# Performance work log

Measured on AMD Instinct MI355X. Metric: run time of the kernel, lower is better.

## Reference

```python
import jax, jax.numpy as jnp
import numpy as np

D_MODEL = 1024
NHEAD = 16
D_K = D_MODEL // NHEAD
CHUNK = 256


def setup_inputs() -> dict:
    key = jax.random.key(0)
    ks = jax.random.split(key, 11)
    S, B = 4096, 4
    inp = {
        "query": jax.random.normal(ks[0], (S, B, D_MODEL), dtype=jnp.float32),
        "key": jax.random.normal(ks[1], (S, B, D_MODEL), dtype=jnp.float32),
        "value": jax.random.normal(ks[2], (S, B, D_MODEL), dtype=jnp.float32),
        # nn.Linear params: y = x @ W.T + b
        "Wq": jax.random.normal(ks[3], (D_MODEL, D_MODEL), dtype=jnp.float32) * 0.02,
        "bq": jnp.zeros((D_MODEL,), dtype=jnp.float32),
        "Wk": jax.random.normal(ks[4], (D_MODEL, D_MODEL), dtype=jnp.float32) * 0.02,
        "bk": jnp.zeros((D_MODEL,), dtype=jnp.float32),
        "Wv": jax.random.normal(ks[5], (D_MODEL, D_MODEL), dtype=jnp.float32) * 0.02,
        "bv": jnp.zeros((D_MODEL,), dtype=jnp.float32),
        "Wo": jax.random.normal(ks[6], (D_MODEL, D_MODEL), dtype=jnp.float32) * 0.02,
        "bo": jnp.zeros((D_MODEL,), dtype=jnp.float32),
    }
    return inp


def _split_heads(x, B):
    # (S, B, D) -> (B, H, S, d_k)
    S = x.shape[0]
    return x.reshape(S, B, NHEAD, D_K).transpose(1, 2, 0, 3)


def reference(query, key, value, Wq, bq, Wk, bk, Wv, bv, Wo, bo):
    S, B, _ = query.shape
    n_chunks = S // CHUNK  # S assumed divisible by CHUNK

    q = _split_heads(query @ Wq.T + bq, B)  # (B,H,S,dk)
    k = _split_heads(key @ Wk.T + bk, B)
    v = _split_heads(value @ Wv.T + bv, B)

    # Block-diagonal attention: softmax is strictly within each chunk.
    qc = q.reshape(B, NHEAD, n_chunks, CHUNK, D_K)
    kc = k.reshape(B, NHEAD, n_chunks, CHUNK, D_K)
    vc = v.reshape(B, NHEAD, n_chunks, CHUNK, D_K)

    scale = 1.0 / np.sqrt(D_K).astype(np.float32)
    scores = jnp.einsum("bhncd,bhnkd->bhnck", qc, kc) * scale  # (B,H,n,C,C)
    probs = jax.nn.softmax(scores, axis=-1)
    out = jnp.einsum("bhnck,bhnkd->bhncd", probs, vc)  # (B,H,n,C,dk)

    # (B,H,S,dk) -> (S,B,H*dk)
    out = out.reshape(B, NHEAD, S, D_K).transpose(2, 0, 1, 3).reshape(S, B, D_MODEL)
    return out @ Wo.T + bo
```

## Files before the change

### kernel.cpp

```cpp
#include <hip/hip_runtime.h>
#include <hip/hip_bf16.h>


namespace {

constexpr int kSeq = 4096, kB = 4, kDm = 1024, kNh = 16, kDk = 64, kChk = 256;
constexpr int kMr = kSeq * kB;
constexpr float kLog2e = 1.44269504088896340736f;

typedef __attribute__((ext_vector_type(8))) short bf16x8;
typedef __attribute__((ext_vector_type(4))) short bf16x4;
typedef __attribute__((ext_vector_type(4))) float f32x4;
typedef __attribute__((ext_vector_type(8))) unsigned short u16x8;
typedef __attribute__((ext_vector_type(4))) unsigned short u16x4;
typedef __attribute__((ext_vector_type(4))) unsigned u32x4;

#define AS1 __attribute__((address_space(1)))
#define AS3 __attribute__((address_space(3)))

__device__ __forceinline__ unsigned short f2bf(float x) {
  union { float f; unsigned u; } v; v.f = x;
  unsigned r = v.u + 0x7fffu + ((v.u >> 16) & 1u);
  return (unsigned short)(r >> 16);
}
__device__ __forceinline__ unsigned cvtpk(float lo, float hi) {
  unsigned r;
  asm("v_cvt_pk_bf16_f32 %0, %1, %2" : "=v"(r) : "v"(lo), "v"(hi));
  return r;
}
__device__ __forceinline__ int swz(int bo) { return bo ^ ((bo >> 3) & 0x70); }

__device__ __forceinline__ f32x4 mfma16x16(bf16x4 a, bf16x4 b, f32x4 c) {
#if __has_builtin(__builtin_amdgcn_mfma_f32_16x16x16bf16_1k)
  return __builtin_amdgcn_mfma_f32_16x16x16bf16_1k(a, b, c, 0, 0, 0);
#else
  asm volatile("v_mfma_f32_16x16x16_bf16 %0, %1, %2, %0\n\ts_nop 4"
               : "+v"(c) : "v"(a), "v"(b));
  return c;
#endif
}

__global__ __launch_bounds__(256) void cvt4(const float* __restrict__ s0,
                                            const float* __restrict__ s1,
                                            const float* __restrict__ s2,
                                            const float* __restrict__ s3,
                                            unsigned short* __restrict__ dst) {
  int i = blockIdx.x * 256 + threadIdx.x;
  int t = i >> 18;
  int j = i & 0x3ffff;
  const float* s = (t == 0) ? s0 : (t == 1) ? s1 : (t == 2) ? s2 : s3;
  f32x4 v = *(const f32x4*)(s + (size_t)j * 4);
  u16x4 o;
  o[0] = f2bf(v[0]); o[1] = f2bf(v[1]); o[2] = f2bf(v[2]); o[3] = f2bf(v[3]);
  *(u16x4*)(dst + (size_t)i * 4) = o;
}

__global__ __launch_bounds__(1024, 4) void gemm_qkv8(
    const float* __restrict__ qf, const float* __restrict__ kf,
    const float* __restrict__ vf, const unsigned short* __restrict__ Wcat,
    const float* __restrict__ bq, const float* __restrict__ bk,
    const float* __restrict__ bv, unsigned short* __restrict__ dst, float sQ) {
  constexpr int K = kDm, nkt = K / 64;
  __shared__ unsigned short sh[65536];
  const int tid = (int)threadIdx.x;
  const int l = tid & 63;
  const int l15 = l & 15, l4 = l >> 4, l7 = l15 & 7;
  const int wid = tid >> 6;
  const int wm = wid >> 2, wn = wid & 3;
  const int bid = (int)blockIdx.x;
  const int xcd = bid & 7, idx = bid >> 3;
  const int rbi = xcd * 8 + (idx & 7);
  const int cbi = idx >> 3;
  const int mat = cbi >> 2, ccol = (cbi & 3) * 256;
  const float* bp = (mat == 0) ? bq : (mat == 1) ? bk : bv;
  const float scale = (mat == 0) ? sQ : 1.0f;
  const float* Ain = (mat == 0) ? qf : (mat == 1) ? kf : vf;
  unsigned short* out = dst + (size_t)mat * kMr * kDm;

  const int ar = tid >> 3, ac = tid & 7;
  const float* gA = Ain + (size_t)(rbi * 256 + ar) * K + ac * 8;
  const int awp = (ac ^ (ar & 7)) * 8;
  const int srow = tid >> 3;
  const int g16 = (tid & 7) ^ (srow & 7);
  const unsigned short* gB = Wcat + (size_t)(cbi * 256 + srow) * K + g16 * 8;
  const int ldsbase = (tid & ~63) * 8;

  auto stageB = [&](int T, int h) {
    const unsigned short* s = gB + (size_t)h * (128 * K) + T * 64;
    unsigned short* d = sh + 32768 + ((T & 1) * 2 + h) * 8192 + ldsbase;
    __builtin_amdgcn_global_load_lds((const AS1 unsigned int*)s, (AS3 unsigned int*)d, 16, 0, 0);
  };
  auto loadA = [&](f32x4* r, int T, int h) {
    const float* s = gA + (size_t)h * (128 * K) + T * 64;
    r[0] = *(const f32x4*)s;
    r[1] = *(const f32x4*)(s + 4);
  };
  auto writeA = [&](const f32x4* r, int T, int h) {
    unsigned short* d = sh + ((T & 1) * 2 + h) * 8192 + ar * 64;
    u32x4 w = {cvtpk(r[0][0], r[0][1]), cvtpk(r[0][2], r[0][3]),
               cvtpk(r[1][0], r[1][1]), cvtpk(r[1][2], r[1][3])};
    *(u32x4*)(d + awp) = w;
  };

  f32x4 acc[4][4] = {};
  f32x4 a0[2], a1[2];
  bf16x8 bfr[4];

  loadA(a0, 0, 0); loadA(a1, 0, 1);
  stageB(0, 0); stageB(0, 1);
  stageB(1, 0); stageB(1, 1);
  writeA(a0, 0, 0); writeA(a1, 0, 1);
  asm volatile("s_waitcnt lgkmcnt(0)" ::: "memory");
  asm volatile("s_waitcnt vmcnt(2)" ::: "memory");
  __builtin_amdgcn_s_barrier();

  for (int it = 0; it < nkt / 2; ++it) {
#pragma unroll
    for (int tt = 0; tt < 2; ++tt) {
      const int T = 2 * it + tt;
      const unsigned short* Asl = sh + (tt * 2 + (wm >> 1)) * 8192;
      const unsigned short* Bsl = sh + 32768 + (tt * 2 + (wn >> 1)) * 8192;
      const int arow0 = (wm & 1) * 64;
      const int brow0 = (wn & 1) * 64;
#pragma unroll
      for (int p = 0; p < 4; ++p) {
        const int kk = p >> 1, mfh = p & 1;
        bf16x8 af[2];
        const int sc = ((kk * 4 + l4) ^ l7) * 8;
        if (mfh == 0) {
#pragma unroll
          for (int nf = 0; nf < 4; ++nf)
            bfr[nf] = *(const bf16x8*)&Bsl[(brow0 + nf * 16 + l15) * 64 + sc];
        }
#pragma unroll
        for (int i = 0; i < 2; ++i)
          af[i] = *(const bf16x8*)&Asl[(arow0 + mfh * 32 + i * 16 + l15) * 64 + sc];
        if (p == 0 && T + 1 < nkt) loadA(a0, T + 1, 0);
        if (p == 1 && T + 1 < nkt) loadA(a1, T + 1, 1);
        if (p == 3) {
          if (T + 2 < nkt) { stageB(T + 2, 0); stageB(T + 2, 1); }
          if (T + 1 < nkt) {
            writeA(a0, T + 1, 0);
            writeA(a1, T + 1, 1);
          }
        }
        __builtin_amdgcn_s_barrier();
        __builtin_amdgcn_s_setprio(1);
#pragma unroll
        for (int i = 0; i < 2; ++i)
#pragma unroll
          for (int nf = 0; nf < 4; ++nf)
            acc[mfh * 2 + i][nf] =
                __builtin_amdgcn_mfma_f32_16x16x32_bf16(af[i], bfr[nf], acc[mfh * 2 + i][nf], 0, 0, 0);
        __builtin_amdgcn_s_setprio(0);
        if (p == 3) {
          asm volatile("s_waitcnt lgkmcnt(0)" ::: "memory");
          if (T + 1 == nkt - 1)
            asm volatile("s_waitcnt vmcnt(0)" ::: "memory");
        }
        __builtin_amdgcn_s_barrier();
      }
    }
  }

#pragma unroll
  for (int mf = 0; mf < 4; ++mf)
#pragma unroll
    for (int nf = 0; nf < 4; ++nf) {
      int col = wn * 64 + nf * 16 + l15;
      float bvv = bp[ccol + col];
      int grpc = col >> 6;
      int c16 = (col & 63) >> 3, pos = col & 7;
      unsigned p01 = cvtpk((acc[mf][nf][0] + bvv) * scale, (acc[mf][nf][1] + bvv) * scale);
      unsigned p23 = cvtpk((acc[mf][nf][2] + bvv) * scale, (acc[mf][nf][3] + bvv) * scale);
      unsigned short ev[4] = {(unsigned short)p01, (unsigned short)(p01 >> 16),
                              (unsigned short)p23, (unsigned short)(p23 >> 16)};
#pragma unroll
      for (int j = 0; j < 4; ++j) {
        int tl = wm * 64 + mf * 16 + l4 * 4 + j;
        int grp = (tl & 3) * 4 + grpc;
        int u = (tl >> 2) * 8 + c16;
        int byte = (grp * 8192 + u * 16 + pos * 2) ^ (((u >> 3) & 7) << 4);
        *(unsigned short*)((char*)sh + byte) = ev[j];
      }
    }
  __syncthreads();
  {
    int inner = tid & 63, grp = tid >> 6;
    int b2 = grp >> 2, hl = grp & 3;
    int h = (cbi & 3) * 4 + hl;
    unsigned short* po = out + ((size_t)(b2 * kNh + h) * kSeq + rbi * 64) * kDk;
#pragma unroll
    for (int i = 0; i < 8; ++i) {
      int u = i * 64 + inner;
      int byte = (grp * 8192 + u * 16) ^ (((u >> 3) & 7) << 4);
      u16x8 v = *(const u16x8*)((const char*)sh + byte);
      *(u16x8*)(po + u * 8) = v;
    }
  }
}

__global__ __launch_bounds__(512, 2) void gemm_o8(const unsigned short* __restrict__ Aw,
                                                  const unsigned short* __restrict__ Bw,
                                                  const float* __restrict__ bias,
                                                  float* __restrict__ Cp) {
  constexpr int K = kDm, nkt = K / 64;
  __shared__ unsigned short sh[65536];
  const int tid = (int)threadIdx.x;
  const int l = tid & 63;
  const int l15 = l & 15, l4 = l >> 4, l7 = l15 & 7;
  const int wid = tid >> 6, wm = wid >> 2, wn = wid & 3, wn1 = wn & 1;
  const int bid = (int)blockIdx.x;
  const int xcd = bid & 7, idx = bid >> 3;
  const int rbi = xcd * 8 + (idx & 7);
  const int cbi = idx >> 3;
  const int rb = rbi * 256, cb = cbi * 256;

  const int srow = tid >> 3;
  const int g16 = (tid & 7) ^ (srow & 7);
  size_t abase[2][2];
#pragma unroll
  for (int h = 0; h < 2; ++h)
#pragma unroll
    for (int i = 0; i < 2; ++i) {
      int t = rb + h * 128 + srow + 64 * i;
      abase[h][i] = ((size_t)((t & 3) * kNh) * kSeq + (t >> 2)) * kDk + g16 * 8;
    }
  const unsigned short* gB = Bw + (size_t)(cb + srow) * K + g16 * 8;
  const int ldsbase = (tid & ~63) * 8;

  auto stageA = [&](int T, int h) {
    unsigned short* d = sh + ((T & 1) * 2 + h) * 8192 + ldsbase;
    size_t ko = (size_t)T * ((size_t)kSeq * kDk);
    __builtin_amdgcn_global_load_lds((const AS1 unsigned int*)(Aw + abase[h][0] + ko),
                                     (AS3 unsigned int*)d, 16, 0, 0);
    __builtin_amdgcn_global_load_lds((const AS1 unsigned int*)(Aw + abase[h][1] + ko),
                                     (AS3 unsigned int*)(d + 4096), 16, 0, 0);
  };
  auto stageB = [&](int T, int h) {
    const unsigned short* s = gB + (size_t)h * (128 * K) + T * 64;
    unsigned short* d = sh + 32768 + ((T & 1) * 2 + h) * 8192 + ldsbase;
    __builtin_amdgcn_global_load_lds((const AS1 unsigned int*)s, (AS3 unsigned int*)d, 16, 0, 0);
    __builtin_amdgcn_global_load_lds((const AS1 unsigned int*)(s + 64 * K),
                                     (AS3 unsigned int*)(d + 4096), 16, 0, 0);
  };

  f32x4 acc[8][4] = {};
  bf16x8 bfr[4];

  stageB(0, 0); stageB(0, 1);
  stageA(0, 0); stageA(0, 1);
  stageB(1, 0); stageB(1, 1);
  asm volatile("s_waitcnt vmcnt(4)" ::: "memory");
  __builtin_amdgcn_s_barrier();

  for (int it = 0; it < nkt / 2; ++it) {
#pragma unroll
    for (int tt = 0; tt < 2; ++tt) {
      const int T = 2 * it + tt;
      const unsigned short* Asl = sh + (tt * 2 + wm) * 8192;
      const unsigned short* Bsl = sh + 32768 + (tt * 2 + (wn >> 1)) * 8192;
#pragma unroll
      for (int p = 0; p < 4; ++p) {
        const int kk = p >> 1, mfh = p & 1;
        bf16x8 af[4];
        const int sc = ((kk * 4 + l4) ^ l7) * 8;
        if (mfh == 0) {
#pragma unroll
          for (int nf = 0; nf < 4; ++nf)
            bfr[nf] = *(const bf16x8*)&Bsl[(wn1 * 64 + nf * 16 + l15) * 64 + sc];
        }
#pragma unroll
        for (int i = 0; i < 4; ++i)
          af[i] = *(const bf16x8*)&Asl[(mfh * 64 + i * 16 + l15) * 64 + sc];
        if (p == 0 && T + 1 < nkt) stageA(T + 1, 0);
        if (p == 1 && T + 1 < nkt) stageA(T + 1, 1);
        if (p == 3 && T + 2 < nkt) { stageB(T + 2, 0); stageB(T + 2, 1); }
        __builtin_amdgcn_s_barrier();
        __builtin_amdgcn_s_setprio(1);
#pragma unroll
        for (int i = 0; i < 4; ++i)
#pragma unroll
          for (int nf = 0; nf < 4; ++nf)
            acc[mfh * 4 + i][nf] =
                __builtin_amdgcn_mfma_f32_16x16x32_bf16(af[i], bfr[nf], acc[mfh * 4 + i][nf], 0, 0, 0);
        __builtin_amdgcn_s_setprio(0);
        if (p == 3 && T + 1 < nkt) {
          if (T + 2 < nkt) asm volatile("s_waitcnt vmcnt(4)" ::: "memory");
          else             asm volatile("s_waitcnt vmcnt(0)" ::: "memory");
        }
        __builtin_amdgcn_s_barrier();
      }
    }
  }

#pragma unroll
  for (int nf = 0; nf < 4; ++nf) {
    int col = cb + wn * 64 + nf * 16 + l15;
    float bvv = bias[col];
#pragma unroll
    for (int mf = 0; mf < 8; ++mf) {
      int row0 = rb + wm * 128 + mf * 16 + l4 * 4;
#pragma unroll
      for (int j = 0; j < 4; ++j)
        Cp[(size_t)(row0 + j) * kDm + col] = acc[mf][nf][j] + bvv;
    }
  }
}

__global__ __launch_bounds__(256) void attn_blkdiag(const unsigned short* __restrict__ qw,
                                                    const unsigned short* __restrict__ kw,
                                                    const unsigned short* __restrict__ vw,
                                                    unsigned short* __restrict__ ow) {
  __shared__ unsigned short Kl[64 * 64];
  __shared__ unsigned short Vt[64 * 64];
  const int tid = (int)threadIdx.x;
  const int w = tid >> 6, l = tid & 63;
  const int l15 = l & 15, l4 = l >> 4;
  const int bid0 = (int)blockIdx.x;
  const int bid = (bid0 & 7) * 256 + (bid0 >> 3);
  const int hf = bid & 1, c = (bid >> 1) & 15, bh = bid >> 5;
  const size_t base = ((size_t)bh * kSeq + c * kChk) * kDk;
  const unsigned short* qp = qw + base + (size_t)hf * 128 * kDk;
  const unsigned short* kp = kw + base;
  const unsigned short* vp = vw + base;

  bf16x8 q[2][2];
#pragma unroll
  for (int m = 0; m < 2; ++m)
#pragma unroll
    for (int kk = 0; kk < 2; ++kk)
      q[m][kk] = *(const bf16x8*)(qp + (w * 32 + m * 16 + l15) * 64 + kk * 32 + l4 * 8);

  float mst[2] = {-1e30f, -1e30f}, lst[2] = {0.f, 0.f};
  f32x4 oacc[2][4] = {};

  const int r = tid >> 2, c0 = (tid & 3) * 16;
  u16x8 kr0, kr1, vr0, vr1;
  {
    const unsigned short* kt = kp + tid * 16;
    kr0 = *(const u16x8*)kt; kr1 = *(const u16x8*)(kt + 8);
    const unsigned short* vt = vp + tid * 16;
    vr0 = *(const u16x8*)vt; vr1 = *(const u16x8*)(vt + 8);
  }

  for (int kb = 0; kb < 4; ++kb) {
    __syncthreads();
    {
      int bo = r * 128 + c0 * 2;
      *(u16x8*)((char*)Kl + swz(bo)) = kr0;
      *(u16x8*)((char*)Kl + swz(bo + 16)) = kr1;
#pragma unroll
      for (int j = 0; j < 8; ++j) {
        *(unsigned short*)((char*)Vt + swz((c0 + j) * 128 + r * 2)) = vr0[j];
        *(unsigned short*)((char*)Vt + swz((c0 + 8 + j) * 128 + r * 2)) = vr1[j];
      }
    }
    __syncthreads();
    if (kb < 3) {
      const unsigned short* kt = kp + (kb + 1) * (64 * kDk) + tid * 16;
      kr0 = *(const u16x8*)kt; kr1 = *(const u16x8*)(kt + 8);
      const unsigned short* vt = vp + (kb + 1) * (64 * kDk) + tid * 16;
      vr0 = *(const u16x8*)vt; vr1 = *(const u16x8*)(vt + 8);
    }

    f32x4 sacc[4][2] = {};
    __builtin_amdgcn_s_setprio(1);
#pragma unroll
    for (int kk = 0; kk < 2; ++kk) {
      bf16x8 kf[4];
#pragma unroll
      for (int kn = 0; kn < 4; ++kn) {
        int bo = (kn * 16 + l15) * 128 + (kk * 32 + l4 * 8) * 2;
        kf[kn] = *(const bf16x8*)((const char*)Kl + swz(bo));
      }
#pragma unroll
      for (int kn = 0; kn < 4; ++kn)
#pragma unroll
        for (int m = 0; m < 2; ++m)
          sacc[kn][m] = __builtin_amdgcn_mfma_f32_16x16x32_bf16(kf[kn], q[m][kk], sacc[kn][m], 0, 0, 0);
    }
    __builtin_amdgcn_s_setprio(0);

    unsigned pw[2][4][2];
    float cbq[2][4];
#pragma unroll
    for (int m = 0; m < 2; ++m) {
      float rm = -1e30f;
#pragma unroll
      for (int kn = 0; kn < 4; ++kn)
#pragma unroll
        for (int j = 0; j < 4; ++j) rm = fmaxf(rm, sacc[kn][m][j]);
      rm = fmaxf(rm, __shfl_xor(rm, 16, 64));
      rm = fmaxf(rm, __shfl_xor(rm, 32, 64));
      float mn = fmaxf(mst[m], rm);
      float corr = exp2f(mst[m] - mn);
      mst[m] = mn;
      float rs = 0.f;
#pragma unroll
      for (int kn = 0; kn < 4; ++kn) {
#pragma unroll
        for (int j = 0; j < 4; ++j) {
          float p = exp2f(sacc[kn][m][j] - mn);
          sacc[kn][m][j] = p;
          rs += p;
        }
        pw[m][kn][0] = cvtpk(sacc[kn][m][0], sacc[kn][m][1]);
        pw[m][kn][1] = cvtpk(sacc[kn][m][2], sacc[kn][m][3]);
      }
      rs += __shfl_xor(rs, 16, 64);
      rs += __shfl_xor(rs, 32, 64);
      lst[m] = lst[m] * corr + rs;
#pragma unroll
      for (int j = 0; j < 4; ++j) cbq[m][j] = __shfl(corr, l4 * 4 + j, 64);
#pragma unroll
      for (int n = 0; n < 4; ++n)
#pragma unroll
        for (int j = 0; j < 4; ++j) oacc[m][n][j] *= cbq[m][j];
    }

    __builtin_amdgcn_s_setprio(1);
#pragma unroll
    for (int kn = 0; kn < 4; ++kn) {
      bf16x4 vf[4];
#pragma unroll
      for (int n = 0; n < 4; ++n) {
        int bo = (n * 16 + l15) * 128 + (kn * 16 + l4 * 4) * 2;
        vf[n] = *(const bf16x4*)((const char*)Vt + swz(bo));
      }
#pragma unroll
      for (int m = 0; m < 2; ++m) {
        union { unsigned u[2]; bf16x4 h; } pk;
        pk.u[0] = pw[m][kn][0]; pk.u[1] = pw[m][kn][1];
#pragma unroll
        for (int n = 0; n < 4; ++n)
          oacc[m][n] = mfma16x16(pk.h, vf[n], oacc[m][n]);
      }
    }
    __builtin_amdgcn_s_setprio(0);
  }

  unsigned short* op = ow + base + (size_t)hf * 128 * kDk;
#pragma unroll
  for (int m = 0; m < 2; ++m) {
    float inv = 1.f / lst[m];
#pragma unroll
    for (int j = 0; j < 4; ++j) {
      float ib = __shfl(inv, l4 * 4 + j, 64);
      int srow = w * 32 + m * 16 + l4 * 4 + j;
#pragma unroll
      for (int n = 0; n < 4; ++n)
        op[(size_t)srow * 64 + n * 16 + l15] = f2bf(oacc[m][n][j] * ib);
    }
  }
}

}

extern "C" void kernel_launch(void* const* d_in, const int* in_sizes, int n_in,
                              void* d_out, int out_size, void* d_ws, size_t ws_size,
                              hipStream_t stream) {
  const float* query = (const float*)d_in[0];
  const float* key   = (const float*)d_in[1];
  const float* value = (const float*)d_in[2];
  const float* Wq = (const float*)d_in[3];
  const float* bq = (const float*)d_in[4];
  const float* Wk = (const float*)d_in[5];
  const float* bk = (const float*)d_in[6];
  const float* Wv = (const float*)d_in[7];
  const float* bv = (const float*)d_in[8];
  const float* Wo = (const float*)d_in[9];
  const float* bo = (const float*)d_in[10];

  const float sQ = 0.125f * kLog2e;

  const size_t wsz = (size_t)kDm * kDm;
  const size_t tsz = (size_t)kMr * kDm;
  unsigned short* wsp = (unsigned short*)d_ws;
  unsigned short* wqb = wsp;
  unsigned short* wob = wqb + 3 * wsz;
  unsigned short* qws = wqb + 4 * wsz;
  unsigned short* kws = qws + tsz;
  unsigned short* vws = kws + tsz;
  unsigned short* aws = vws + tsz;

  const size_t need = (4 * wsz + 4 * tsz) * 2;
  if (ws_size < need) return;

  cvt4<<<dim3(4096), dim3(256), 0, stream>>>(Wq, Wk, Wv, Wo, wqb);
  gemm_qkv8<<<dim3(768), dim3(1024), 0, stream>>>(query, key, value, wqb,
                                                  bq, bk, bv, qws, sQ);
  attn_blkdiag<<<dim3(2048), 256, 0, stream>>>(qws, kws, vws, aws);
  gemm_o8<<<dim3(256), dim3(512), 0, stream>>>(aws, wob, bo, (float*)d_out);
}
```

Before: 242.1 us.

## Prefetch QKV A-tiles two steps ahead; run output GEMM with 16 waves

In the QKV GEMM, fp32 A-tile register loads now go two k-steps ahead using two alternating register sets, with vmcnt waits adjusted to match, so global load latency gets more time to hide. The output GEMM moves from 512 to 1024 threads per block, and each wave now owns a 64x64 sub-tile instead of 128x64. That cuts per-thread accumulators and loads per stage to raise wave-level parallelism. The costs are more registers held in the QKV kernel, and tighter register limits plus more barrier participants in the output GEMM.

```diff
diff --git a/kernel.cpp b/kernel.cpp
--- a/kernel.cpp
+++ b/kernel.cpp
@@ -103,13 +103,14 @@
   };
 
   f32x4 acc[4][4] = {};
-  f32x4 a0[2], a1[2];
+  f32x4 s0h0[2], s0h1[2], s1h0[2], s1h1[2];
   bf16x8 bfr[4];
 
-  loadA(a0, 0, 0); loadA(a1, 0, 1);
+  loadA(s0h0, 0, 0); loadA(s0h1, 0, 1);
+  loadA(s1h0, 1, 0); loadA(s1h1, 1, 1);
   stageB(0, 0); stageB(0, 1);
   stageB(1, 0); stageB(1, 1);
-  writeA(a0, 0, 0); writeA(a1, 0, 1);
+  writeA(s0h0, 0, 0); writeA(s0h1, 0, 1);
   asm volatile("s_waitcnt lgkmcnt(0)" ::: "memory");
   asm volatile("s_waitcnt vmcnt(2)" ::: "memory");
   __builtin_amdgcn_s_barrier();
@@ -135,13 +136,13 @@
 #pragma unroll
         for (int i = 0; i < 2; ++i)
           af[i] = *(const bf16x8*)&Asl[(arow0 + mfh * 32 + i * 16 + l15) * 64 + sc];
-        if (p == 0 && T + 1 < nkt) loadA(a0, T + 1, 0);
-        if (p == 1 && T + 1 < nkt) loadA(a1, T + 1, 1);
+        if (p == 0 && T + 2 < nkt) loadA(tt == 0 ? s0h0 : s1h0, T + 2, 0);
+        if (p == 1 && T + 2 < nkt) loadA(tt == 0 ? s0h1 : s1h1, T + 2, 1);
         if (p == 3) {
           if (T + 2 < nkt) { stageB(T + 2, 0); stageB(T + 2, 1); }
           if (T + 1 < nkt) {
-            writeA(a0, T + 1, 0);
-            writeA(a1, T + 1, 1);
+            writeA(tt == 0 ? s1h0 : s0h0, T + 1, 0);
+            writeA(tt == 0 ? s1h1 : s0h1, T + 1, 1);
           }
         }
         __builtin_amdgcn_s_barrier();
@@ -155,8 +156,10 @@
         __builtin_amdgcn_s_setprio(0);
         if (p == 3) {
           asm volatile("s_waitcnt lgkmcnt(0)" ::: "memory");
-          if (T + 1 == nkt - 1)
-            asm volatile("s_waitcnt vmcnt(0)" ::: "memory");
+          if (T + 1 < nkt) {
+            if (T + 2 < nkt) asm volatile("s_waitcnt vmcnt(6)" ::: "memory");
+            else             asm volatile("s_waitcnt vmcnt(0)" ::: "memory");
+          }
         }
         __builtin_amdgcn_s_barrier();
       }
@@ -200,16 +203,17 @@
   }
 }
 
-__global__ __launch_bounds__(512, 2) void gemm_o8(const unsigned short* __restrict__ Aw,
-                                                  const unsigned short* __restrict__ Bw,
-                                                  const float* __restrict__ bias,
-                                                  float* __restrict__ Cp) {
+__global__ __launch_bounds__(1024, 4) void gemm_o8(const unsigned short* __restrict__ Aw,
+                                                   const unsigned short* __restrict__ Bw,
+                                                   const float* __restrict__ bias,
+                                                   float* __restrict__ Cp) {
   constexpr int K = kDm, nkt = K / 64;
   __shared__ unsigned short sh[65536];
   const int tid = (int)threadIdx.x;
   const int l = tid & 63;
   const int l15 = l & 15, l4 = l >> 4, l7 = l15 & 7;
-  const int wid = tid >> 6, wm = wid >> 2, wn = wid & 3, wn1 = wn & 1;
+  const int wid = tid >> 6;
+  const int wm = wid >> 2, wn = wid & 3;
   const int bid = (int)blockIdx.x;
   const int xcd = bid & 7, idx = bid >> 3;
   const int rbi = xcd * 8 + (idx & 7);
@@ -218,75 +222,71 @@
 
   const int srow = tid >> 3;
   const int g16 = (tid & 7) ^ (srow & 7);
-  size_t abase[2][2];
-#pragma unroll
-  for (int h = 0; h < 2; ++h)
-#pragma unroll
-    for (int i = 0; i < 2; ++i) {
-      int t = rb + h * 128 + srow + 64 * i;
-      abase[h][i] = ((size_t)((t & 3) * kNh) * kSeq + (t >> 2)) * kDk + g16 * 8;
-    }
+  size_t abase[2];
+#pragma unroll
+  for (int h = 0; h < 2; ++h) {
+    int t = rb + h * 128 + srow;
+    abase[h] = ((size_t)((t & 3) * kNh) * kSeq + (t >> 2)) * kDk + g16 * 8;
+  }
   const unsigned short* gB = Bw + (size_t)(cb + srow) * K + g16 * 8;
   const int ldsbase = (tid & ~63) * 8;
 
   auto stageA = [&](int T, int h) {
     unsigned short* d = sh + ((T & 1) * 2 + h) * 8192 + ldsbase;
     size_t ko = (size_t)T * ((size_t)kSeq * kDk);
-    __builtin_amdgcn_global_load_lds((const AS1 unsigned int*)(Aw + abase[h][0] + ko),
+    __builtin_amdgcn_global_load_lds((const AS1 unsigned int*)(Aw + abase[h] + ko),
                                      (AS3 unsigned int*)d, 16, 0, 0);
-    __builtin_amdgcn_global_load_lds((const AS1 unsigned int*)(Aw + abase[h][1] + ko),
-                                     (AS3 unsigned int*)(d + 4096), 16, 0, 0);
   };
   auto stageB = [&](int T, int h) {
     const unsigned short* s = gB + (size_t)h * (128 * K) + T * 64;
     unsigned short* d = sh + 32768 + ((T & 1) * 2 + h) * 8192 + ldsbase;
     __builtin_amdgcn_global_load_lds((const AS1 unsigned int*)s, (AS3 unsigned int*)d, 16, 0, 0);
-    __builtin_amdgcn_global_load_lds((const AS1 unsigned int*)(s + 64 * K),
-                                     (AS3 unsigned int*)(d + 4096), 16, 0, 0);
   };
 
-  f32x4 acc[8][4] = {};
+  f32x4 acc[4][4] = {};
   bf16x8 bfr[4];
 
   stageB(0, 0); stageB(0, 1);
   stageA(0, 0); stageA(0, 1);
   stageB(1, 0); stageB(1, 1);
-  asm volatile("s_waitcnt vmcnt(4)" ::: "memory");
+  asm volatile("s_waitcnt vmcnt(2)" ::: "memory");
   __builtin_amdgcn_s_barrier();
 
   for (int it = 0; it < nkt / 2; ++it) {
 #pragma unroll
     for (int tt = 0; tt < 2; ++tt) {
       const int T = 2 * it + tt;
-      const unsigned short* Asl = sh + (tt * 2 + wm) * 8192;
+      const unsigned short* Asl = sh + (tt * 2 + (wm >> 1)) * 8192;
       const unsigned short* Bsl = sh + 32768 + (tt * 2 + (wn >> 1)) * 8192;
+      const int arow0 = (wm & 1) * 64;
+      const int brow0 = (wn & 1) * 64;
 #pragma unroll
       for (int p = 0; p < 4; ++p) {
         const int kk = p >> 1, mfh = p & 1;
-        bf16x8 af[4];
+        bf16x8 af[2];
         const int sc = ((kk * 4 + l4) ^ l7) * 8;
         if (mfh == 0) {
 #pragma unroll
           for (int nf = 0; nf < 4; ++nf)
-            bfr[nf] = *(const bf16x8*)&Bsl[(wn1 * 64 + nf * 16 + l15) * 64 + sc];
-        }
-#pragma unroll
-        for (int i = 0; i < 4; ++i)
-          af[i] = *(const bf16x8*)&Asl[(mfh * 64 + i * 16 + l15) * 64 + sc];
+            bfr[nf] = *(const bf16x8*)&Bsl[(brow0 + nf * 16 + l15) * 64 + sc];
+        }
+#pragma unroll
+        for (int i = 0; i < 2; ++i)
+          af[i] = *(const bf16x8*)&Asl[(arow0 + mfh * 32 + i * 16 + l15) * 64 + sc];
         if (p == 0 && T + 1 < nkt) stageA(T + 1, 0);
         if (p == 1 && T + 1 < nkt) stageA(T + 1, 1);
         if (p == 3 && T + 2 < nkt) { stageB(T + 2, 0); stageB(T + 2, 1); }
         __builtin_amdgcn_s_barrier();
         __builtin_amdgcn_s_setprio(1);
 #pragma unroll
-        for (int i = 0; i < 4; ++i)
+        for (int i = 0; i < 2; ++i)
 #pragma unroll
           for (int nf = 0; nf < 4; ++nf)
-            acc[mfh * 4 + i][nf] =
-                __builtin_amdgcn_mfma_f32_16x16x32_bf16(af[i], bfr[nf], acc[mfh * 4 + i][nf], 0, 0, 0);
+            acc[mfh * 2 + i][nf] =
+                __builtin_amdgcn_mfma_f32_16x16x32_bf16(af[i], bfr[nf], acc[mfh * 2 + i][nf], 0, 0, 0);
         __builtin_amdgcn_s_setprio(0);
         if (p == 3 && T + 1 < nkt) {
-          if (T + 2 < nkt) asm volatile("s_waitcnt vmcnt(4)" ::: "memory");
+          if (T + 2 < nkt) asm volatile("s_waitcnt vmcnt(2)" ::: "memory");
           else             asm volatile("s_waitcnt vmcnt(0)" ::: "memory");
         }
         __builtin_amdgcn_s_barrier();
@@ -299,8 +299,8 @@
     int col = cb + wn * 64 + nf * 16 + l15;
     float bvv = bias[col];
 #pragma unroll
-    for (int mf = 0; mf < 8; ++mf) {
-      int row0 = rb + wm * 128 + mf * 16 + l4 * 4;
+    for (int mf = 0; mf < 4; ++mf) {
+      int row0 = rb + wm * 64 + mf * 16 + l4 * 4;
 #pragma unroll
       for (int j = 0; j < 4; ++j)
         Cp[(size_t)(row0 + j) * kDm + col] = acc[mf][nf][j] + bvv;
@@ -491,5 +491,5 @@
   gemm_qkv8<<<dim3(768), dim3(1024), 0, stream>>>(query, key, value, wqb,
                                                   bq, bk, bv, qws, sQ);
   attn_blkdiag<<<dim3(2048), 256, 0, stream>>>(qws, kws, vws, aws);
-  gemm_o8<<<dim3(256), dim3(512), 0, stream>>>(aws, wob, bo, (float*)d_out);
-}
+  gemm_o8<<<dim3(256), dim3(1024), 0, stream>>>(aws, wob, bo, (float*)d_out);
+}
```

After: 405.8 us. 1.68x slower.
